# Kernel tuning notes

Hardware: AMD Instinct MI355X
Metric: run time of the kernel (lower is better)

## Reference

```python
import jax, jax.numpy as jnp
import numpy as np

B, S = 1, 1024
V_SZ, D, L, H, DK, DV = 50304, 768, 12, 24, 32, 32
EPS = 1e-5


def layernorm(x, g, b):
    m = jnp.mean(x, axis=-1, keepdims=True)
    v = jnp.mean((x - m) ** 2, axis=-1, keepdims=True)
    return (x - m) * jax.lax.rsqrt(v + EPS) * g + b


def setup_inputs() -> dict:
    key = jax.random.key(0)
    ks = jax.random.split(key, 8)
    s = 0.02
    qkv_out = H * (DK + DK + DV)
    return {
        "token_ids": jax.random.randint(ks[0], (B, S), 0, V_SZ),
        "embed_w": (jax.random.uniform(ks[1], (V_SZ, D), minval=-1.0, maxval=1.0) / np.float32(np.sqrt(D))).astype(jnp.float32),
        "pos_w": jax.random.normal(ks[2], (D, 2 * D), dtype=jnp.float32) * s,
        "pos_b": jnp.zeros((2 * D,), jnp.float32),
        "ln1_g": jnp.ones((L, D), jnp.float32),
        "ln1_b": jnp.zeros((L, D), jnp.float32),
        "qkv_w": jax.random.normal(ks[3], (L, D, qkv_out), dtype=jnp.float32) * s,
        "qkv_b": jnp.zeros((L, qkv_out), jnp.float32),
        "ff_w1": jax.random.normal(ks[4], (L, H * DV, 2 * D), dtype=jnp.float32) * s,
        "ff_b1": jnp.zeros((L, 2 * D), jnp.float32),
        "ff_w2": jax.random.normal(ks[5], (L, D, D), dtype=jnp.float32) * s,
        "lnf_g": jnp.ones((D,), jnp.float32),
        "lnf_b": jnp.zeros((D,), jnp.float32),
    }


def _embed_position(x, pos_w, pos_b):
    # Heinsen log-linear recurrence (arXiv:2311.06281), using_prev_context=False.
    h = x @ pos_w + pos_b                     # [B,S,2D]
    log_coeffs = jax.nn.log_sigmoid(h[..., :D])
    logits = h[..., D:]
    a_star = jnp.pad(jnp.cumsum(log_coeffs, axis=1), ((0, 0), (1, 0), (0, 0)))  # [B,S+1,D]
    prepended = jnp.pad(logits, ((0, 0), (1, 0), (0, 0)))                        # logit0 = 0
    rec = a_star + jax.lax.cumlogsumexp(prepended - a_star, axis=1)
    return x + rec[:, 1:, :]


def _layer(x, p):
    g1, b1, wqkv, bqkv, w1, bb1, w2 = p
    y = layernorm(x, g1, b1) @ wqkv + bqkv                  # [B,S,H*(2DK+DV)]
    y = y.reshape(B, S, H, DK + DK + DV).transpose(0, 2, 1, 3)  # [B,H,S,.]
    Q, K, V = y[..., :DK], y[..., DK:2 * DK], y[..., 2 * DK:]
    # Heinsen log-domain causal attention (arXiv:2404.05843)
    H_S = jax.lax.cumlogsumexp(K[..., :, None] + V[..., None, :], axis=2)  # [B,H,S,DK,DV]
    H_Z = jax.lax.cumlogsumexp(K, axis=2)                                   # [B,H,S,DK]
    log_S = jax.nn.logsumexp(Q[..., None] + H_S, axis=-2)                   # [B,H,S,DV]
    log_Z = jax.nn.logsumexp(Q + H_Z, axis=-1, keepdims=True)               # [B,H,S,1]
    att = (log_S - log_Z).transpose(0, 2, 1, 3).reshape(B, S, H * DV)
    z = att @ w1 + bb1                                       # [B,S,2D]
    z = z[..., :D] * jax.nn.sigmoid(z[..., D:])              # GLU(dim=-1)
    z = z @ w2
    return x + z, None


def reference(token_ids, embed_w, pos_w, pos_b, ln1_g, ln1_b, qkv_w, qkv_b, ff_w1, ff_b1, ff_w2, lnf_g, lnf_b):
    x = embed_w[token_ids]                                   # [B,S,D]
    x = _embed_position(x, pos_w, pos_b)
    x, _ = jax.lax.scan(_layer, x, (ln1_g, ln1_b, qkv_w, qkv_b, ff_w1, ff_b1, ff_w2))
    x = layernorm(x, lnf_g, lnf_b)
    return x @ embed_w.T                                     # [B,S,V_SZ]
```

## Files before the change

### kernel.cpp

```cpp
#include <hip/hip_runtime.h>
#include <math.h>

#define S 1024
#define D 768
#define L 12
#define NH 24
#define QKV_OUT 2304
#define FF1_OUT 1536
#define V_SZ 50304

typedef unsigned short u16;
typedef __attribute__((ext_vector_type(8))) short bf16x8;
typedef __attribute__((ext_vector_type(4))) float f32x4;

__device__ __forceinline__ u16 f2bf(float x) {
    unsigned u = __float_as_uint(x);
    u += 0x7fffu + ((u >> 16) & 1u);
    return (u16)(u >> 16);
}

__device__ __forceinline__ void async_copy16(const void* g, void* l) {
    __builtin_amdgcn_global_load_lds(
        (const __attribute__((address_space(1))) unsigned int*)g,
        (__attribute__((address_space(3))) unsigned int*)l, 16, 0, 0);
}

__global__ __launch_bounds__(256) void embed_kernel(
    const int* __restrict__ tok, const float* __restrict__ ew,
    float* __restrict__ x, u16* __restrict__ xb) {
    int t = blockIdx.x;
    int id = tok[t];
    const float* src = ew + (size_t)id * D;
    for (int d = threadIdx.x; d < D; d += 256) {
        float v = src[d];
        x[(size_t)t * D + d] = v;
        xb[(size_t)t * D + d] = f2bf(v);
    }
}

__global__ __launch_bounds__(256) void cvt_bf16_kernel(
    const float* __restrict__ in, u16* __restrict__ out) {
    size_t i = ((size_t)blockIdx.x * 256 + threadIdx.x) * 8;
    float4 a = *(const float4*)(in + i);
    float4 b = *(const float4*)(in + i + 4);
    uint4 o;
    o.x = (unsigned)f2bf(a.x) | ((unsigned)f2bf(a.y) << 16);
    o.y = (unsigned)f2bf(a.z) | ((unsigned)f2bf(a.w) << 16);
    o.z = (unsigned)f2bf(b.x) | ((unsigned)f2bf(b.y) << 16);
    o.w = (unsigned)f2bf(b.z) | ((unsigned)f2bf(b.w) << 16);
    *(uint4*)(out + i) = o;
}

__global__ __launch_bounds__(256) void pos_scan_kernel(
    const float* __restrict__ h, float* __restrict__ x) {
    const int d = blockIdx.x;
    const int tid = threadIdx.x;
    float a[4], b[4];
    #pragma unroll
    for (int i = 0; i < 4; ++i) {
        int t = tid * 4 + i;
        float g  = h[(size_t)t * FF1_OUT + d];
        float lg = h[(size_t)t * FF1_OUT + D + d];
        a[i] = 1.f / (1.f + __expf(-g));
        b[i] = __expf(lg);
    }
    float A = ((a[0] * a[1]) * a[2]) * a[3];
    float B = ((b[0] * a[1] + b[1]) * a[2] + b[2]) * a[3] + b[3];

    __shared__ float sA[256], sB[256];
    sA[tid] = A; sB[tid] = B;
    __syncthreads();
    #pragma unroll
    for (int off = 1; off < 256; off <<= 1) {
        float selfA = sA[tid], selfB = sB[tid];
        float pA = 1.f, pB = 0.f;
        if (tid >= off) { pA = sA[tid - off]; pB = sB[tid - off]; }
        __syncthreads();
        sA[tid] = pA * selfA;
        sB[tid] = pB * selfA + selfB;
        __syncthreads();
    }
    float R = 1.f;
    if (tid > 0) R = sA[tid - 1] + sB[tid - 1];
    #pragma unroll
    for (int i = 0; i < 4; ++i) {
        R = R * a[i] + b[i];
        x[(size_t)(tid * 4 + i) * D + d] += __logf(R);
    }
}

__global__ __launch_bounds__(256) void ln_kernel(
    const float* __restrict__ in, const float* __restrict__ g,
    const float* __restrict__ b, u16* __restrict__ out) {
    int row = blockIdx.x;
    int tid = threadIdx.x;
    const float* p = in + (size_t)row * D;
    float v0 = p[tid], v1 = p[tid + 256], v2 = p[tid + 512];

    __shared__ float red[8];
    float s = v0 + v1 + v2;
    #pragma unroll
    for (int o = 32; o > 0; o >>= 1) s += __shfl_down(s, o, 64);
    int wave = tid >> 6, lane = tid & 63;
    if (lane == 0) red[wave] = s;
    __syncthreads();
    float mean = (red[0] + red[1] + red[2] + red[3]) * (1.f / (float)D);

    float d0 = v0 - mean, d1 = v1 - mean, d2 = v2 - mean;
    float ss = d0 * d0 + d1 * d1 + d2 * d2;
    #pragma unroll
    for (int o = 32; o > 0; o >>= 1) ss += __shfl_down(ss, o, 64);
    if (lane == 0) red[4 + wave] = ss;
    __syncthreads();
    float var = (red[4] + red[5] + red[6] + red[7]) * (1.f / (float)D);
    float rstd = rsqrtf(var + 1e-5f);

    u16* o = out + (size_t)row * D;
    o[tid]       = f2bf(d0 * rstd * g[tid]       + b[tid]);
    o[tid + 256] = f2bf(d1 * rstd * g[tid + 256] + b[tid + 256]);
    o[tid + 512] = f2bf(d2 * rstd * g[tid + 512] + b[tid + 512]);
}

__global__ __launch_bounds__(256) void wconv_kernel(
    const float* __restrict__ W, u16* __restrict__ WT, int N) {
    __shared__ float tile[32][33];
    const int z = blockIdx.z;
    W  += (size_t)z * 768 * N;
    WT += (size_t)z * N * 768;
    const int n0 = blockIdx.x * 32, k0 = blockIdx.y * 32;
    const int t = threadIdx.x;
    const int r = t >> 3, c4 = (t & 7) * 4;
    float4 v = *(const float4*)(W + (size_t)(k0 + r) * N + n0 + c4);
    tile[r][c4] = v.x; tile[r][c4 + 1] = v.y; tile[r][c4 + 2] = v.z; tile[r][c4 + 3] = v.w;
    __syncthreads();
    ushort4 o;
    o.x = f2bf(tile[c4][r]);     o.y = f2bf(tile[c4 + 1][r]);
    o.z = f2bf(tile[c4 + 2][r]); o.w = f2bf(tile[c4 + 3][r]);
    *(ushort4*)(WT + (size_t)(n0 + r) * 768 + k0 + c4) = o;
}

template <bool SWAP>
__global__ __launch_bounds__(256) void gemm_bf16_kernel(
    const u16* __restrict__ A, const u16* __restrict__ B,
    const float* __restrict__ bias, const float* __restrict__ Cin,
    float* __restrict__ C, int N) {
    constexpr int K = 768;
    constexpr int NT = K / 32;
    __shared__ __align__(16) u16 As[2][128 * 32];
    __shared__ __align__(16) u16 Bs[2][128 * 32];
    const int tid = threadIdx.x;
    const int w = tid >> 6, lane = tid & 63;
    const int m0 = (SWAP ? blockIdx.x : blockIdx.y) * 128;
    const int n0 = (SWAP ? blockIdx.y : blockIdx.x) * 128;
    const int wm = (w >> 1) * 64, wn = (w & 1) * 64;

    f32x4 acc[4][4] = {};

    const int rA = w * 32 + (lane >> 2);
    const int cA = (lane & 3) * 8;
    const int frow = lane & 15;
    const int fko = (lane >> 4) * 8;

    const u16* gA = A + (size_t)(m0 + rA) * K + cA;
    const u16* gB = B + (size_t)(n0 + rA) * K + cA;

    async_copy16(gA, (char*)As[0] + w * 2048);
    async_copy16(gA + (size_t)16 * K, (char*)As[0] + w * 2048 + 1024);
    async_copy16(gB, (char*)Bs[0] + w * 2048);
    async_copy16(gB + (size_t)16 * K, (char*)Bs[0] + w * 2048 + 1024);
    __syncthreads();

    int cur = 0;
    for (int t = 0; t < NT; ++t) {
        if (t + 1 < NT) {
            const u16* a1 = gA + (t + 1) * 32;
            const u16* b1 = gB + (t + 1) * 32;
            async_copy16(a1, (char*)As[cur ^ 1] + w * 2048);
            async_copy16(a1 + (size_t)16 * K, (char*)As[cur ^ 1] + w * 2048 + 1024);
            async_copy16(b1, (char*)Bs[cur ^ 1] + w * 2048);
            async_copy16(b1 + (size_t)16 * K, (char*)Bs[cur ^ 1] + w * 2048 + 1024);
        }
        bf16x8 af[4], bfr[4];
        #pragma unroll
        for (int i = 0; i < 4; ++i)
            af[i] = *(const bf16x8*)(As[cur] + (wm + i * 16 + frow) * 32 + fko);
        #pragma unroll
        for (int j = 0; j < 4; ++j)
            bfr[j] = *(const bf16x8*)(Bs[cur] + (wn + j * 16 + frow) * 32 + fko);
        #pragma unroll
        for (int i = 0; i < 4; ++i)
            #pragma unroll
            for (int j = 0; j < 4; ++j)
                acc[i][j] = __builtin_amdgcn_mfma_f32_16x16x32_bf16(af[i], bfr[j], acc[i][j], 0, 0, 0);
        __syncthreads();
        cur ^= 1;
    }

    const int crow = wm + (lane >> 4) * 4;
    const int ccol = wn + (lane & 15);
    #pragma unroll
    for (int j = 0; j < 4; ++j) {
        int col = n0 + ccol + j * 16;
        float bj = bias ? bias[col] : 0.f;
        #pragma unroll
        for (int i = 0; i < 4; ++i) {
            #pragma unroll
            for (int r = 0; r < 4; ++r) {
                int row = m0 + crow + i * 16 + r;
                size_t off = (size_t)row * N + col;
                float v = acc[i][j][r] + bj;
                if (Cin) v += Cin[off];
                C[off] = v;
            }
        }
    }
}

__global__ __launch_bounds__(256) void gemm_f32b_kernel(
    const u16* __restrict__ A, const float* __restrict__ B,
    const float* __restrict__ bias, const float* __restrict__ Cin,
    float* __restrict__ C, int N) {
    constexpr int K = 768;
    __shared__ __align__(16) u16 As[128 * 32];
    __shared__ __align__(16) u16 Bs[128 * 32];
    const int tid = threadIdx.x;
    const int w = tid >> 6, lane = tid & 63;
    const int m0 = blockIdx.y * 128, n0 = blockIdx.x * 128;
    const int wm = (w >> 1) * 64, wn = (w & 1) * 64;

    f32x4 acc[4][4] = {};

    const int rA = w * 32 + (lane >> 2);
    const int cA = (lane & 3) * 8;
    const int frow = lane & 15;
    const int fko = (lane >> 4) * 8;

    for (int k0 = 0; k0 < K; k0 += 32) {
        {
            const u16* g0 = A + (size_t)(m0 + rA) * K + k0 + cA;
            async_copy16(g0, (char*)As + w * 2048);
            async_copy16(g0 + (size_t)16 * K, (char*)As + w * 2048 + 1024);
        }
        {
            const int r = tid >> 1, half = tid & 1;
            const float* src = B + (size_t)(n0 + r) * K + k0 + half * 16;
            float4 v0 = *(const float4*)(src);
            float4 v1 = *(const float4*)(src + 4);
            float4 v2 = *(const float4*)(src + 8);
            float4 v3 = *(const float4*)(src + 12);
            unsigned p0 = (unsigned)f2bf(v0.x) | ((unsigned)f2bf(v0.y) << 16);
            unsigned p1 = (unsigned)f2bf(v0.z) | ((unsigned)f2bf(v0.w) << 16);
            unsigned p2 = (unsigned)f2bf(v1.x) | ((unsigned)f2bf(v1.y) << 16);
            unsigned p3 = (unsigned)f2bf(v1.z) | ((unsigned)f2bf(v1.w) << 16);
            unsigned p4 = (unsigned)f2bf(v2.x) | ((unsigned)f2bf(v2.y) << 16);
            unsigned p5 = (unsigned)f2bf(v2.z) | ((unsigned)f2bf(v2.w) << 16);
            unsigned p6 = (unsigned)f2bf(v3.x) | ((unsigned)f2bf(v3.y) << 16);
            unsigned p7 = (unsigned)f2bf(v3.z) | ((unsigned)f2bf(v3.w) << 16);
            u16* dst = Bs + r * 32 + half * 16;
            *(uint4*)(dst)     = make_uint4(p0, p1, p2, p3);
            *(uint4*)(dst + 8) = make_uint4(p4, p5, p6, p7);
        }
        __syncthreads();

        bf16x8 af[4], bfr[4];
        #pragma unroll
        for (int i = 0; i < 4; ++i)
            af[i] = *(const bf16x8*)(As + (wm + i * 16 + frow) * 32 + fko);
        #pragma unroll
        for (int j = 0; j < 4; ++j)
            bfr[j] = *(const bf16x8*)(Bs + (wn + j * 16 + frow) * 32 + fko);
        #pragma unroll
        for (int i = 0; i < 4; ++i)
            #pragma unroll
            for (int j = 0; j < 4; ++j)
                acc[i][j] = __builtin_amdgcn_mfma_f32_16x16x32_bf16(af[i], bfr[j], acc[i][j], 0, 0, 0);
        __syncthreads();
    }

    const int crow = wm + (lane >> 4) * 4;
    const int ccol = wn + (lane & 15);
    #pragma unroll
    for (int j = 0; j < 4; ++j) {
        int col = n0 + ccol + j * 16;
        float bj = bias ? bias[col] : 0.f;
        #pragma unroll
        for (int i = 0; i < 4; ++i) {
            #pragma unroll
            for (int r = 0; r < 4; ++r) {
                int row = m0 + crow + i * 16 + r;
                size_t off = (size_t)row * N + col;
                float v = acc[i][j][r] + bj;
                if (Cin) v += Cin[off];
                C[off] = v;
            }
        }
    }
}

__global__ __launch_bounds__(256) void attn_kernel(
    const float* __restrict__ y, u16* __restrict__ att) {
    const int tb = blockIdx.x, head = blockIdx.y;
    const int tid = threadIdx.x, w = tid >> 6, lane = tid & 63;
    const int q = lane >> 4, cl = lane & 15;
    const int t0 = tb * 64;

    __shared__ __align__(16) u16 Qs[64 * 32];
    __shared__ __align__(16) u16 Ks[64 * 32];
    __shared__ __align__(16) u16 Vt[32 * 64];
    __shared__ __align__(16) u16 As[4][16 * 64];
    u16* As_w = As[w];

    bf16x8 ones8;
    #pragma unroll
    for (int i = 0; i < 8; ++i) ones8[i] = (short)0x3F80;

    f32x4 accO[2] = {};
    f32x4 accZ = {};

    #pragma unroll
    for (int i = 0; i < 2; ++i) {
        int e = tid + i * 256;
        int row = e >> 3, c4 = (e & 7) * 4;
        float4 v = *(const float4*)(y + (size_t)(t0 + row) * QKV_OUT + head * 96 + c4);
        ushort4 o;
        o.x = f2bf(__expf(v.x)); o.y = f2bf(__expf(v.y));
        o.z = f2bf(__expf(v.z)); o.w = f2bf(__expf(v.w));
        *(ushort4*)(Qs + row * 32 + c4) = o;
    }

    for (int sb = 0; sb <= tb; ++sb) {
        const int s0 = sb * 64;
        #pragma unroll
        for (int i = 0; i < 2; ++i) {
            int e = tid + i * 256;
            int row = e >> 3, c4 = (e & 7) * 4;
            const float* src = y + (size_t)(s0 + row) * QKV_OUT + head * 96;
            float4 kv = *(const float4*)(src + 32 + c4);
            ushort4 o;
            o.x = f2bf(__expf(kv.x)); o.y = f2bf(__expf(kv.y));
            o.z = f2bf(__expf(kv.z)); o.w = f2bf(__expf(kv.w));
            *(ushort4*)(Ks + row * 32 + c4) = o;
            float4 vv = *(const float4*)(src + 64 + c4);
            float ev[4] = {__expf(vv.x), __expf(vv.y), __expf(vv.z), __expf(vv.w)};
            #pragma unroll
            for (int n = 0; n < 4; ++n) {
                int j = c4 + n;
                Vt[j * 64 + (((row >> 4) ^ (j & 3)) * 16) + (row & 15)] = f2bf(ev[n]);
            }
        }
        __syncthreads();

        bf16x8 af_q = *(const bf16x8*)(Qs + (w * 16 + cl) * 32 + q * 8);
        f32x4 aqk[4];
        #pragma unroll
        for (int nt = 0; nt < 4; ++nt) {
            bf16x8 bk = *(const bf16x8*)(Ks + (nt * 16 + cl) * 32 + q * 8);
            aqk[nt] = __builtin_amdgcn_mfma_f32_16x16x32_bf16(af_q, bk, (f32x4){0.f, 0.f, 0.f, 0.f}, 0, 0, 0);
        }
        #pragma unroll
        for (int nt = 0; nt < 4; ++nt) {
            #pragma unroll
            for (int reg = 0; reg < 4; ++reg) {
                int r = q * 4 + reg;
                int tg = t0 + w * 16 + r;
                int cg = s0 + nt * 16 + cl;
                float v = (cg <= tg) ? aqk[nt][reg] : 0.f;
                As_w[r * 64 + ((nt ^ q) * 16) + cl] = f2bf(v);
            }
        }
        bf16x8 af_a[2];
        #pragma unroll
        for (int kt = 0; kt < 2; ++kt) {
            int blk = (kt * 2 + (q >> 1)) ^ (cl >> 2);
            af_a[kt] = *(const bf16x8*)(As_w + cl * 64 + blk * 16 + (q & 1) * 8);
        }
        #pragma unroll
        for (int kt = 0; kt < 2; ++kt)
            accZ = __builtin_amdgcn_mfma_f32_16x16x32_bf16(af_a[kt], ones8, accZ, 0, 0, 0);
        #pragma unroll
        for (int nt = 0; nt < 2; ++nt) {
            #pragma unroll
            for (int kt = 0; kt < 2; ++kt) {
                int j = nt * 16 + cl;
                int blk = (kt * 2 + (q >> 1)) ^ (j & 3);
                bf16x8 bv = *(const bf16x8*)(Vt + j * 64 + blk * 16 + (q & 1) * 8);
                accO[nt] = __builtin_amdgcn_mfma_f32_16x16x32_bf16(af_a[kt], bv, accO[nt], 0, 0, 0);
            }
        }
        __syncthreads();
    }

    #pragma unroll
    for (int nt = 0; nt < 2; ++nt) {
        #pragma unroll
        for (int reg = 0; reg < 4; ++reg) {
            int t = t0 + w * 16 + q * 4 + reg;
            int j = nt * 16 + cl;
            att[(size_t)t * D + head * 32 + j] = f2bf(__logf(accO[nt][reg]) - __logf(accZ[reg]));
        }
    }
}

__global__ __launch_bounds__(256) void glu_kernel(
    const float* __restrict__ z, u16* __restrict__ zg) {
    int idx = blockIdx.x * 256 + threadIdx.x;
    int t = idx / D, d = idx - t * D;
    float a = z[(size_t)t * FF1_OUT + d];
    float g = z[(size_t)t * FF1_OUT + D + d];
    zg[idx] = f2bf(a * (1.f / (1.f + __expf(-g))));
}

extern "C" void kernel_launch(void* const* d_in, const int* in_sizes, int n_in,
                              void* d_out, int out_size, void* d_ws, size_t ws_size,
                              hipStream_t stream) {
    const int*   tok     = (const int*)d_in[0];
    const float* embed_w = (const float*)d_in[1];
    const float* pos_w   = (const float*)d_in[2];
    const float* pos_b   = (const float*)d_in[3];
    const float* ln1_g   = (const float*)d_in[4];
    const float* ln1_b   = (const float*)d_in[5];
    const float* qkv_w   = (const float*)d_in[6];
    const float* qkv_b   = (const float*)d_in[7];
    const float* ff_w1   = (const float*)d_in[8];
    const float* ff_b1   = (const float*)d_in[9];
    const float* ff_w2   = (const float*)d_in[10];
    const float* lnf_g   = (const float*)d_in[11];
    const float* lnf_b   = (const float*)d_in[12];
    float* out = (float*)d_out;

    char* base = (char*)d_ws;
    float* X    = (float*)(base);
    u16*   XB   = (u16*)  (base + 3145728);
    float* Y    = (float*)(base + 4718592);
    u16*   LNX  = (u16*)  (base + 14155776);
    u16*   ATT  = (u16*)  (base + 15728640);
    u16*   ZG   = (u16*)  (base + 17301504);
    u16*   posT = (u16*)  (base + 18874368);
    u16*   qkvT = (u16*)  (base + 21233664);
    u16*   ff1T = (u16*)  (base + 63700992);
    u16*   ff2T = (u16*)  (base + 92012544);
    u16*   EBW  = (u16*)  (base + 106168320);
    const bool bf16_head = ws_size >= (size_t)106168320 + 77266944;

    wconv_kernel<<<dim3(48, 24, 1),  256, 0, stream>>>(pos_w, posT, 1536);
    wconv_kernel<<<dim3(72, 24, 12), 256, 0, stream>>>(qkv_w, qkvT, 2304);
    wconv_kernel<<<dim3(48, 24, 12), 256, 0, stream>>>(ff_w1, ff1T, 1536);
    wconv_kernel<<<dim3(24, 24, 12), 256, 0, stream>>>(ff_w2, ff2T, 768);

    embed_kernel<<<S, 256, 0, stream>>>(tok, embed_w, X, XB);

    gemm_bf16_kernel<false><<<dim3(12, 8), 256, 0, stream>>>(XB, posT, pos_b, nullptr, Y, FF1_OUT);
    pos_scan_kernel<<<D, 256, 0, stream>>>(Y, X);

    for (int l = 0; l < L; ++l) {
        ln_kernel<<<S, 256, 0, stream>>>(X, ln1_g + (size_t)l * D, ln1_b + (size_t)l * D, LNX);
        gemm_bf16_kernel<false><<<dim3(18, 8), 256, 0, stream>>>(
            LNX, qkvT + (size_t)l * QKV_OUT * 768, qkv_b + (size_t)l * QKV_OUT, nullptr, Y, QKV_OUT);
        attn_kernel<<<dim3(16, NH), 256, 0, stream>>>(Y, ATT);
        gemm_bf16_kernel<false><<<dim3(12, 8), 256, 0, stream>>>(
            ATT, ff1T + (size_t)l * FF1_OUT * 768, ff_b1 + (size_t)l * FF1_OUT, nullptr, Y, FF1_OUT);
        glu_kernel<<<(S * D) / 256, 256, 0, stream>>>(Y, ZG);
        gemm_bf16_kernel<false><<<dim3(6, 8), 256, 0, stream>>>(
            ZG, ff2T + (size_t)l * D * 768, nullptr, X, X, D);
    }

    ln_kernel<<<S, 256, 0, stream>>>(X, lnf_g, lnf_b, LNX);
    if (bf16_head) {
        cvt_bf16_kernel<<<18864, 256, 0, stream>>>(embed_w, EBW);
        gemm_bf16_kernel<true><<<dim3(8, 393), 256, 0, stream>>>(LNX, EBW, nullptr, nullptr, out, V_SZ);
    } else {
        gemm_f32b_kernel<<<dim3(393, 8), 256, 0, stream>>>(LNX, embed_w, nullptr, nullptr, out, V_SZ);
    }
}
```

Baseline: 1.926 ms.

## Precompute exp(K),exp(V) once per layer; XCD-swizzle LM head; single-buffer GEMM

Adds a kernel that computes bf16 exp(K) and exp(V) once per token per layer, so the causal attention blocks no longer recompute exponentials for every earlier key block. The LM-head GEMM switches to a 1D grid with an XCD-aware remap so that neighbouring N tiles land on the same chiplet for L2 reuse. The GEMM loses its double-buffered LDS prefetch and now loads each k-tile synchronously before computing it, which frees LDS but exposes memory latency. EKV reuses the EBW workspace region, which is only written later by the head conversion.

Measured after the change: 1.913 ms. About the same (-0.7%).

```diff
diff --git a/kernel.cpp b/kernel.cpp
--- a/kernel.cpp
+++ b/kernel.cpp
@@ -139,19 +139,27 @@
     *(ushort4*)(WT + (size_t)(n0 + r) * 768 + k0 + c4) = o;
 }
 
-template <bool SWAP>
+template <bool XSWZ>
 __global__ __launch_bounds__(256) void gemm_bf16_kernel(
     const u16* __restrict__ A, const u16* __restrict__ B,
     const float* __restrict__ bias, const float* __restrict__ Cin,
     float* __restrict__ C, int N) {
     constexpr int K = 768;
-    constexpr int NT = K / 32;
-    __shared__ __align__(16) u16 As[2][128 * 32];
-    __shared__ __align__(16) u16 Bs[2][128 * 32];
+    __shared__ __align__(16) u16 As[128 * 32];
+    __shared__ __align__(16) u16 Bs[128 * 32];
     const int tid = threadIdx.x;
     const int w = tid >> 6, lane = tid & 63;
-    const int m0 = (SWAP ? blockIdx.x : blockIdx.y) * 128;
-    const int n0 = (SWAP ? blockIdx.y : blockIdx.x) * 128;
+    int m0, n0;
+    if (XSWZ) {
+        const int lid = blockIdx.x;
+        const int xcd = lid & 7, local = lid >> 3;
+        const int work = xcd * 393 + local;
+        n0 = (work >> 3) * 128;
+        m0 = (work & 7) * 128;
+    } else {
+        m0 = blockIdx.y * 128;
+        n0 = blockIdx.x * 128;
+    }
     const int wm = (w >> 1) * 64, wn = (w & 1) * 64;
 
     f32x4 acc[4][4] = {};
@@ -161,39 +169,32 @@
     const int frow = lane & 15;
     const int fko = (lane >> 4) * 8;
 
-    const u16* gA = A + (size_t)(m0 + rA) * K + cA;
-    const u16* gB = B + (size_t)(n0 + rA) * K + cA;
-
-    async_copy16(gA, (char*)As[0] + w * 2048);
-    async_copy16(gA + (size_t)16 * K, (char*)As[0] + w * 2048 + 1024);
-    async_copy16(gB, (char*)Bs[0] + w * 2048);
-    async_copy16(gB + (size_t)16 * K, (char*)Bs[0] + w * 2048 + 1024);
-    __syncthreads();
-
-    int cur = 0;
-    for (int t = 0; t < NT; ++t) {
-        if (t + 1 < NT) {
-            const u16* a1 = gA + (t + 1) * 32;
-            const u16* b1 = gB + (t + 1) * 32;
-            async_copy16(a1, (char*)As[cur ^ 1] + w * 2048);
-            async_copy16(a1 + (size_t)16 * K, (char*)As[cur ^ 1] + w * 2048 + 1024);
-            async_copy16(b1, (char*)Bs[cur ^ 1] + w * 2048);
-            async_copy16(b1 + (size_t)16 * K, (char*)Bs[cur ^ 1] + w * 2048 + 1024);
-        }
+    for (int k0 = 0; k0 < K; k0 += 32) {
+        {
+            const u16* g0 = A + (size_t)(m0 + rA) * K + k0 + cA;
+            async_copy16(g0, (char*)As + w * 2048);
+            async_copy16(g0 + (size_t)16 * K, (char*)As + w * 2048 + 1024);
+        }
+        {
+            const u16* g0 = B + (size_t)(n0 + rA) * K + k0 + cA;
+            async_copy16(g0, (char*)Bs + w * 2048);
+            async_copy16(g0 + (size_t)16 * K, (char*)Bs + w * 2048 + 1024);
+        }
+        __syncthreads();
+
         bf16x8 af[4], bfr[4];
         #pragma unroll
         for (int i = 0; i < 4; ++i)
-            af[i] = *(const bf16x8*)(As[cur] + (wm + i * 16 + frow) * 32 + fko);
+            af[i] = *(const bf16x8*)(As + (wm + i * 16 + frow) * 32 + fko);
         #pragma unroll
         for (int j = 0; j < 4; ++j)
-            bfr[j] = *(const bf16x8*)(Bs[cur] + (wn + j * 16 + frow) * 32 + fko);
+            bfr[j] = *(const bf16x8*)(Bs + (wn + j * 16 + frow) * 32 + fko);
         #pragma unroll
         for (int i = 0; i < 4; ++i)
             #pragma unroll
             for (int j = 0; j < 4; ++j)
                 acc[i][j] = __builtin_amdgcn_mfma_f32_16x16x32_bf16(af[i], bfr[j], acc[i][j], 0, 0, 0);
         __syncthreads();
-        cur ^= 1;
     }
 
     const int crow = wm + (lane >> 4) * 4;
@@ -297,8 +298,27 @@
     }
 }
 
+__global__ __launch_bounds__(256) void ekv_kernel(
+    const float* __restrict__ y, u16* __restrict__ ekv) {
+    const int t = blockIdx.x;
+    #pragma unroll
+    for (int i = 0; i < 2; ++i) {
+        int e = threadIdx.x + i * 256;
+        int off = e * 4;
+        if (off < NH * 64) {
+            int h = off >> 6, c = off & 63;
+            float4 v = *(const float4*)(y + (size_t)t * QKV_OUT + h * 96 + 32 + c);
+            ushort4 o;
+            o.x = f2bf(__expf(v.x)); o.y = f2bf(__expf(v.y));
+            o.z = f2bf(__expf(v.z)); o.w = f2bf(__expf(v.w));
+            *(ushort4*)(ekv + (size_t)t * (NH * 64) + off) = o;
+        }
+    }
+}
+
 __global__ __launch_bounds__(256) void attn_kernel(
-    const float* __restrict__ y, u16* __restrict__ att) {
+    const float* __restrict__ y, const u16* __restrict__ ekv,
+    u16* __restrict__ att) {
     const int tb = blockIdx.x, head = blockIdx.y;
     const int tid = threadIdx.x, w = tid >> 6, lane = tid & 63;
     const int q = lane >> 4, cl = lane & 15;
@@ -334,18 +354,15 @@
         for (int i = 0; i < 2; ++i) {
             int e = tid + i * 256;
             int row = e >> 3, c4 = (e & 7) * 4;
-            const float* src = y + (size_t)(s0 + row) * QKV_OUT + head * 96;
-            float4 kv = *(const float4*)(src + 32 + c4);
-            ushort4 o;
-            o.x = f2bf(__expf(kv.x)); o.y = f2bf(__expf(kv.y));
-            o.z = f2bf(__expf(kv.z)); o.w = f2bf(__expf(kv.w));
-            *(ushort4*)(Ks + row * 32 + c4) = o;
-            float4 vv = *(const float4*)(src + 64 + c4);
-            float ev[4] = {__expf(vv.x), __expf(vv.y), __expf(vv.z), __expf(vv.w)};
+            const u16* src = ekv + (size_t)(s0 + row) * (NH * 64) + head * 64;
+            ushort4 k4 = *(const ushort4*)(src + c4);
+            *(ushort4*)(Ks + row * 32 + c4) = k4;
+            ushort4 v4 = *(const ushort4*)(src + 32 + c4);
+            u16 vv[4] = {v4.x, v4.y, v4.z, v4.w};
             #pragma unroll
             for (int n = 0; n < 4; ++n) {
                 int j = c4 + n;
-                Vt[j * 64 + (((row >> 4) ^ (j & 3)) * 16) + (row & 15)] = f2bf(ev[n]);
+                Vt[j * 64 + (((row >> 4) ^ (j & 3)) * 16) + (row & 15)] = vv[n];
             }
         }
         __syncthreads();
@@ -440,6 +457,7 @@
     u16*   ff1T = (u16*)  (base + 63700992);
     u16*   ff2T = (u16*)  (base + 92012544);
     u16*   EBW  = (u16*)  (base + 106168320);
+    u16*   EKV  = (u16*)  (base + 106168320);
     const bool bf16_head = ws_size >= (size_t)106168320 + 77266944;
 
     wconv_kernel<<<dim3(48, 24, 1),  256, 0, stream>>>(pos_w, posT, 1536);
@@ -456,7 +474,8 @@
         ln_kernel<<<S, 256, 0, stream>>>(X, ln1_g + (size_t)l * D, ln1_b + (size_t)l * D, LNX);
         gemm_bf16_kernel<false><<<dim3(18, 8), 256, 0, stream>>>(
             LNX, qkvT + (size_t)l * QKV_OUT * 768, qkv_b + (size_t)l * QKV_OUT, nullptr, Y, QKV_OUT);
-        attn_kernel<<<dim3(16, NH), 256, 0, stream>>>(Y, ATT);
+        ekv_kernel<<<S, 256, 0, stream>>>(Y, EKV);
+        attn_kernel<<<dim3(16, NH), 256, 0, stream>>>(Y, EKV, ATT);
         gemm_bf16_kernel<false><<<dim3(12, 8), 256, 0, stream>>>(
             ATT, ff1T + (size_t)l * FF1_OUT * 768, ff_b1 + (size_t)l * FF1_OUT, nullptr, Y, FF1_OUT);
         glu_kernel<<<(S * D) / 256, 256, 0, stream>>>(Y, ZG);
@@ -467,7 +486,7 @@
     ln_kernel<<<S, 256, 0, stream>>>(X, lnf_g, lnf_b, LNX);
     if (bf16_head) {
         cvt_bf16_kernel<<<18864, 256, 0, stream>>>(embed_w, EBW);
-        gemm_bf16_kernel<true><<<dim3(8, 393), 256, 0, stream>>>(LNX, EBW, nullptr, nullptr, out, V_SZ);
+        gemm_bf16_kernel<true><<<dim3(3144), 256, 0, stream>>>(LNX, EBW, nullptr, nullptr, out, V_SZ);
     } else {
         gemm_f32b_kernel<<<dim3(393, 8), 256, 0, stream>>>(LNX, embed_w, nullptr, nullptr, out, V_SZ);
     }
```
